# Optimization experiments

Measured on AMD Instinct MI355X. Metric: run time of the kernel, lower is better.

Reference implementation:

```python
import jax, jax.numpy as jnp
import numpy as np

ALPHA = 0.2  # LeakyReLU negative slope

B, K, F = 64, 100, 128   # batch, window_size (=num_nodes), n_features
E = 2 * K                 # embed_dim*2 = 200 (embed_dim defaults to window_size)


def setup_inputs() -> dict:
    key = jax.random.key(0)
    k1, k2, k3, k4, k5 = jax.random.split(key, 5)
    x = jax.random.normal(k1, (B, K, F), dtype=jnp.float32)
    # lin: Linear(2F -> E); store weight as (2F, E) so projection is x @ W
    W = jax.random.normal(k2, (2 * F, E), dtype=jnp.float32) * (1.0 / np.sqrt(2 * F))
    b = jax.random.normal(k3, (E,), dtype=jnp.float32) * 0.01
    # attention vector a: (E, 1) in torch; use (E,)
    a = jax.random.normal(k4, (E,), dtype=jnp.float32) * (1.414 / np.sqrt(E))
    bias = jax.random.normal(k5, (K, K), dtype=jnp.float32) * 0.01
    return {"x": x, "W": W, "b": b, "a": a, "bias": bias}


def reference(x, W, b, a, bias):
    F_ = x.shape[-1]
    # lin(concat(left, right)) == left @ W[:F] + right @ W[F:] + b;
    # compute the two projections once each instead of materializing the
    # (B, K, K, 2F) pairwise concat tensor.
    left_p = jnp.einsum('bkf,fe->bke', x, W[:F_])    # (B, K, E)
    right_p = jnp.einsum('bkf,fe->bke', x, W[F_:])   # (B, K, E)
    pre = left_p[:, :, None, :] + right_p[:, None, :, :] + b  # (B, K, K, E)
    act = jnp.where(pre > 0, pre, ALPHA * pre)                # LeakyReLU
    e = jnp.einsum('bije,e->bij', act, a) + bias              # (B, K, K)
    attention = jax.nn.softmax(e, axis=2)
    h = jax.nn.sigmoid(jnp.einsum('bij,bjf->bif', attention, x))  # (B, K, F)
    return h
```

## Files before the change

kernel.cpp:

```cpp
#include <hip/hip_runtime.h>

typedef _Float16 half_t;
typedef _Float16 h2 __attribute__((ext_vector_type(2)));
typedef unsigned int uint32;

#define K_ 100
#define F_ 128
#define E_ 200

#if defined(__has_builtin)
#if __has_builtin(__builtin_amdgcn_fdot2)
#define FDOT2(a,b,c) __builtin_amdgcn_fdot2((a),(b),(c),false)
#endif
#endif
#ifndef FDOT2
#define FDOT2(a,b,c) fmaf((float)(a).y,(float)(b).y, fmaf((float)(a).x,(float)(b).x,(c)))
#endif

__device__ __forceinline__ h2 bch2(uint32 u){ return __builtin_bit_cast(h2,u); }
__device__ __forceinline__ uint32 pkh2(float a, float b){
  h2 p; p.x=(half_t)a; p.y=(half_t)b; return __builtin_bit_cast(uint32,p);
}

#define LH_OFF 0
#define RH_OFF 640000
#define AH_OFF 1280000
#define WT_OFF 1280128
#define AL_OFF 1305728
#define AR_OFF 1312128
#define XJ_OFF 1318528

__global__ __launch_bounds__(256) void k_wt(
    const float* __restrict__ W, const float* __restrict__ avec,
    uint32* __restrict__ ws)
{
  const int t  = threadIdx.x;
  const int e0 = (int)blockIdx.x * 8;
  __shared__ float wtf[256 * 9];

  for (int u = t; u < 2048; u += 256) {
    int f = u >> 3, ec = u & 7;
    wtf[f * 9 + ec] = W[(size_t)f * E_ + e0 + ec];
  }
  if (blockIdx.x == 0 && t < 100)
    ws[AH_OFF + t] = pkh2(avec[2*t], avec[2*t+1]);
  __syncthreads();

  for (int u = t; u < 1024; u += 256) {
    int col16 = u >> 6, f2 = u & 63;
    int side = col16 >> 3, el = col16 & 7;
    int cu = side * 200 + e0 + el;
    int fbase = side * 128;
    ws[WT_OFF + (size_t)cu * 64 + f2] =
        pkh2(wtf[(fbase + 2*f2) * 9 + el], wtf[(fbase + 2*f2 + 1) * 9 + el]);
  }
}

__global__ __launch_bounds__(256) void k_proj(
    const float* __restrict__ x, const float* __restrict__ bvec,
    uint32* __restrict__ ws)
{
  const int t  = threadIdx.x;
  const int r0 = (int)blockIdx.x * 10;

  __shared__ __align__(16) uint32 xsh[10 * 64];
  __shared__ float red[20][100];

  for (int u = t; u < 640; u += 256) {
    int row = u >> 6, f2 = u & 63;
    const float* xp = x + (size_t)(r0 + row) * F_ + 2 * f2;
    xsh[row * 64 + f2] = pkh2(xp[0], xp[1]);
  }
  __syncthreads();

  for (int u = t; u < 640; u += 256) {
    int f = u & 127, lp = u >> 7;
    uint32 u0 = xsh[(2*lp)     * 64 + (f >> 1)];
    uint32 u1 = xsh[(2*lp + 1) * 64 + (f >> 1)];
    int sh = (f & 1) * 16;
    uint32 h0 = (u0 >> sh) & 0xffffu;
    uint32 h1 = (u1 >> sh) & 0xffffu;
    ws[XJ_OFF + (size_t)(r0/2 + lp) * 128 + f] = h0 | (h1 << 16);
  }

  if (t < 200) {
    const uint32* wt0 = ws + WT_OFF + (size_t)(2 * t) * 64;
    const uint32* wt1 = wt0 + 64;
    float acc0[10], acc1[10];
    #pragma unroll
    for (int r = 0; r < 10; ++r) { acc0[r] = 0.f; acc1[r] = 0.f; }
    #pragma unroll
    for (int q = 0; q < 16; ++q) {
      uint4 w0 = *(const uint4*)(wt0 + 4 * q);
      uint4 w1 = *(const uint4*)(wt1 + 4 * q);
      #pragma unroll
      for (int r = 0; r < 10; ++r) {
        uint4 xq = *(const uint4*)(xsh + r * 64 + 4 * q);
        acc0[r] = FDOT2(bch2(xq.x), bch2(w0.x), acc0[r]);
        acc0[r] = FDOT2(bch2(xq.y), bch2(w0.y), acc0[r]);
        acc0[r] = FDOT2(bch2(xq.z), bch2(w0.z), acc0[r]);
        acc0[r] = FDOT2(bch2(xq.w), bch2(w0.w), acc0[r]);
        acc1[r] = FDOT2(bch2(xq.x), bch2(w1.x), acc1[r]);
        acc1[r] = FDOT2(bch2(xq.y), bch2(w1.y), acc1[r]);
        acc1[r] = FDOT2(bch2(xq.z), bch2(w1.z), acc1[r]);
        acc1[r] = FDOT2(bch2(xq.w), bch2(w1.w), acc1[r]);
      }
    }
    const bool isR = (t >= 100);
    const int e2 = isR ? (t - 100) : t;
    if (isR) {
      float b0 = bvec[2 * e2], b1 = bvec[2 * e2 + 1];
      #pragma unroll
      for (int r = 0; r < 10; ++r) { acc0[r] += b0; acc1[r] += b1; }
    }
    h2 a2 = bch2(ws[AH_OFF + e2]);
    uint32* dst = ws + (isR ? RH_OFF : LH_OFF);
    #pragma unroll
    for (int r = 0; r < 10; ++r) {
      uint32 pr = pkh2(acc0[r], acc1[r]);
      dst[(size_t)(r0 + r) * 100 + e2] = pr;
      red[(isR ? 10 : 0) + r][e2] = FDOT2(a2, bch2(pr), 0.f);
    }
  }
  __syncthreads();

  if (t < 20) {
    float s = 0.f;
    const float* rp = red[t];
    for (int k = 0; k < 100; ++k) s += rp[k];
    float* dstf = (float*)(ws + (t >= 10 ? AR_OFF : AL_OFF));
    dstf[r0 + (t % 10)] = s;
  }
}

#define STEP(lu, au, r0u, r1u, r2u, r3u)                                   \
  do {                                                                     \
    h2 a2 = bch2(au); h2 l2 = bch2(lu); h2 mm;                             \
    mm = __builtin_elementwise_min(l2 + bch2(r0u), z2); acc[0] = FDOT2(a2, mm, acc[0]); \
    mm = __builtin_elementwise_min(l2 + bch2(r1u), z2); acc[1] = FDOT2(a2, mm, acc[1]); \
    mm = __builtin_elementwise_min(l2 + bch2(r2u), z2); acc[2] = FDOT2(a2, mm, acc[2]); \
    mm = __builtin_elementwise_min(l2 + bch2(r3u), z2); acc[3] = FDOT2(a2, mm, acc[3]); \
  } while (0)

#define RPAD 104
#define LPAD 108

__global__ __launch_bounds__(256) void k_main(
    const float* __restrict__ x, const float* __restrict__ bias,
    const uint32* __restrict__ ws, float* __restrict__ out)
{
  const int t  = threadIdx.x;
  const int i0 = (int)blockIdx.x * 10;
  const int b  = (int)blockIdx.y;

  __shared__ __align__(16) uint32 Rsh[100 * RPAD];
  __shared__ __align__(16) uint32 Lsh[10 * LPAD];
  __shared__ uint32 Ash[100];
  __shared__ float  att[10 * 100];
  __shared__ uint32 att2[10 * 50];
  __shared__ float  scratch[256];
  __shared__ float  rowmax[10], rowinv[10];

  const bool act = (t < 250);
  const int ti = act ? (t % 10) : 0;
  const int tj = act ? (t / 10) : 0;

  {
    const uint32* Rb = ws + RH_OFF + (size_t)b * K_ * 100;
    for (int u = t; u < 2500; u += 256) {
      int row = u / 25, c4 = (u % 25) * 4;
      *(uint4*)(&Rsh[row * RPAD + c4]) = *(const uint4*)(Rb + (size_t)row * 100 + c4);
    }
    const uint32* Lb = ws + LH_OFF + (size_t)(b * K_ + i0) * 100;
    if (t < 250) {
      int row = t / 25, c4 = (t % 25) * 4;
      *(uint4*)(&Lsh[row * LPAD + c4]) = *(const uint4*)(Lb + (size_t)row * 100 + c4);
    }
    if (t < 100) Ash[t] = ws[AH_OFF + t];
  }
  __syncthreads();

  float acc[4] = {0.f,0.f,0.f,0.f};
  h2 z2; z2.x = (half_t)0; z2.y = (half_t)0;

  if (act) {
    const uint32* Lp  = Lsh + ti * LPAD;
    const uint32* Rp0 = Rsh + tj * RPAD;
    const uint32* Rp1 = Rsh + (tj + 25) * RPAD;
    const uint32* Rp2 = Rsh + (tj + 50) * RPAD;
    const uint32* Rp3 = Rsh + (tj + 75) * RPAD;
    #pragma unroll 5
    for (int q = 0; q < 25; ++q) {
      uint4 Lq = *(const uint4*)(Lp  + 4*q);
      uint4 Aq = *(const uint4*)(Ash + 4*q);
      uint4 R0q = *(const uint4*)(Rp0 + 4*q);
      uint4 R1q = *(const uint4*)(Rp1 + 4*q);
      uint4 R2q = *(const uint4*)(Rp2 + 4*q);
      uint4 R3q = *(const uint4*)(Rp3 + 4*q);
      STEP(Lq.x, Aq.x, R0q.x, R1q.x, R2q.x, R3q.x);
      STEP(Lq.y, Aq.y, R0q.y, R1q.y, R2q.y, R3q.y);
      STEP(Lq.z, Aq.z, R0q.z, R1q.z, R2q.z, R3q.z);
      STEP(Lq.w, Aq.w, R0q.w, R1q.w, R2q.w, R3q.w);
    }
  }

  float v[4];
  if (act) {
    const float* ALf = (const float*)(ws + AL_OFF);
    const float* ARf = (const float*)(ws + AR_OFF);
    float al = ALf[b*K_ + i0 + ti];
    #pragma unroll
    for (int s = 0; s < 4; ++s) {
      int j = tj + 25*s;
      float lv = al + ARf[b*K_ + j] + bias[(i0 + ti)*K_ + j] - 0.8f*acc[s];
      v[s] = fminf(fmaxf(lv, -30000.f), 30000.f);
    }
  }

  {
    float m = -3.0e38f;
    if (act) {
      #pragma unroll
      for (int s = 0; s < 4; ++s) m = fmaxf(m, v[s]);
    }
    scratch[t] = m;
    __syncthreads();
    if (t < 10) {
      float mm = scratch[t];
      for (int k = 1; k < 25; ++k) mm = fmaxf(mm, scratch[t + 10*k]);
      rowmax[t] = mm;
    }
    __syncthreads();
    float ssum = 0.f;
    if (act) {
      float m2 = rowmax[ti];
      #pragma unroll
      for (int s = 0; s < 4; ++s) ssum += __expf(v[s] - m2);
    }
    scratch[t] = ssum;
    __syncthreads();
    if (t < 10) {
      float s2 = 0.f;
      for (int k = 0; k < 25; ++k) s2 += scratch[t + 10*k];
      rowinv[t] = 1.f / s2;
    }
    __syncthreads();
  }
  if (act) {
    float m = rowmax[ti], inv = rowinv[ti];
    #pragma unroll
    for (int s = 0; s < 4; ++s)
      att[ti*K_ + tj + 25*s] = __expf(v[s] - m) * inv;
  }
  __syncthreads();
  for (int u = t; u < 500; u += 256) {
    int i = u / 50, jp = u - i*50;
    att2[i*50 + jp] = pkh2(att[i*K_ + 2*jp], att[i*K_ + 2*jp + 1]);
  }
  __syncthreads();

  {
    const int f = t & 127, ig = t >> 7;
    const uint32* XJ = ws + XJ_OFF + (size_t)(b*50) * 128;
    float z[5];
    #pragma unroll
    for (int m = 0; m < 5; ++m) z[m] = 0.f;
    for (int jp = 0; jp < 50; ++jp) {
      h2 xv = bch2(XJ[jp*128 + f]);
      #pragma unroll
      for (int m = 0; m < 5; ++m) {
        h2 av = bch2(att2[(ig*5 + m)*50 + jp]);
        z[m] = FDOT2(av, xv, z[m]);
      }
    }
    #pragma unroll
    for (int m = 0; m < 5; ++m) {
      int i = ig*5 + m;
      out[(size_t)(b*K_ + i0 + i)*F_ + f] = 1.f / (1.f + __expf(-z[m]));
    }
  }
}

extern "C" void kernel_launch(void* const* d_in, const int* in_sizes, int n_in,
                              void* d_out, int out_size, void* d_ws, size_t ws_size,
                              hipStream_t stream)
{
  const float* x    = (const float*)d_in[0];
  const float* W    = (const float*)d_in[1];
  const float* bvec = (const float*)d_in[2];
  const float* avec = (const float*)d_in[3];
  const float* bias = (const float*)d_in[4];
  float* out  = (float*)d_out;
  uint32* ws  = (uint32*)d_ws;

  k_wt  <<<dim3(25),     dim3(256), 0, stream>>>(W, avec, ws);
  k_proj<<<dim3(640),    dim3(256), 0, stream>>>(x, bvec, ws);
  k_main<<<dim3(10, 64), dim3(256), 0, stream>>>(x, bias, ws, out);
}
```

Baseline: 101.8 us.

## Fuse weight prep, projection and attention into one persistent kernel with grid barrier

```diff
diff --git a/kernel.cpp b/kernel.cpp
--- a/kernel.cpp
+++ b/kernel.cpp
@@ -7,6 +7,7 @@
 #define K_ 100
 #define F_ 128
 #define E_ 200
+#define NBLK 640u
 
 #if defined(__has_builtin)
 #if __has_builtin(__builtin_amdgcn_fdot2)
@@ -22,115 +23,33 @@
   h2 p; p.x=(half_t)a; p.y=(half_t)b; return __builtin_bit_cast(uint32,p);
 }
 
-#define LH_OFF 0
-#define RH_OFF 640000
-#define AH_OFF 1280000
-#define WT_OFF 1280128
-#define AL_OFF 1305728
-#define AR_OFF 1312128
-#define XJ_OFF 1318528
-
-__global__ __launch_bounds__(256) void k_wt(
-    const float* __restrict__ W, const float* __restrict__ avec,
-    uint32* __restrict__ ws)
+#define RH_OFF  0
+#define AR_WOFF 640000
+#define XJ_WOFF 646400
+
+__device__ unsigned gbar_cnt = 0;
+__device__ unsigned gbar_gen = 0;
+
+__device__ __forceinline__ void grid_barrier()
 {
-  const int t  = threadIdx.x;
-  const int e0 = (int)blockIdx.x * 8;
-  __shared__ float wtf[256 * 9];
-
-  for (int u = t; u < 2048; u += 256) {
-    int f = u >> 3, ec = u & 7;
-    wtf[f * 9 + ec] = W[(size_t)f * E_ + e0 + ec];
-  }
-  if (blockIdx.x == 0 && t < 100)
-    ws[AH_OFF + t] = pkh2(avec[2*t], avec[2*t+1]);
-  __syncthreads();
-
-  for (int u = t; u < 1024; u += 256) {
-    int col16 = u >> 6, f2 = u & 63;
-    int side = col16 >> 3, el = col16 & 7;
-    int cu = side * 200 + e0 + el;
-    int fbase = side * 128;
-    ws[WT_OFF + (size_t)cu * 64 + f2] =
-        pkh2(wtf[(fbase + 2*f2) * 9 + el], wtf[(fbase + 2*f2 + 1) * 9 + el]);
-  }
-}
-
-__global__ __launch_bounds__(256) void k_proj(
-    const float* __restrict__ x, const float* __restrict__ bvec,
-    uint32* __restrict__ ws)
-{
-  const int t  = threadIdx.x;
-  const int r0 = (int)blockIdx.x * 10;
-
-  __shared__ __align__(16) uint32 xsh[10 * 64];
-  __shared__ float red[20][100];
-
-  for (int u = t; u < 640; u += 256) {
-    int row = u >> 6, f2 = u & 63;
-    const float* xp = x + (size_t)(r0 + row) * F_ + 2 * f2;
-    xsh[row * 64 + f2] = pkh2(xp[0], xp[1]);
-  }
-  __syncthreads();
-
-  for (int u = t; u < 640; u += 256) {
-    int f = u & 127, lp = u >> 7;
-    uint32 u0 = xsh[(2*lp)     * 64 + (f >> 1)];
-    uint32 u1 = xsh[(2*lp + 1) * 64 + (f >> 1)];
-    int sh = (f & 1) * 16;
-    uint32 h0 = (u0 >> sh) & 0xffffu;
-    uint32 h1 = (u1 >> sh) & 0xffffu;
-    ws[XJ_OFF + (size_t)(r0/2 + lp) * 128 + f] = h0 | (h1 << 16);
-  }
-
-  if (t < 200) {
-    const uint32* wt0 = ws + WT_OFF + (size_t)(2 * t) * 64;
-    const uint32* wt1 = wt0 + 64;
-    float acc0[10], acc1[10];
-    #pragma unroll
-    for (int r = 0; r < 10; ++r) { acc0[r] = 0.f; acc1[r] = 0.f; }
-    #pragma unroll
-    for (int q = 0; q < 16; ++q) {
-      uint4 w0 = *(const uint4*)(wt0 + 4 * q);
-      uint4 w1 = *(const uint4*)(wt1 + 4 * q);
-      #pragma unroll
-      for (int r = 0; r < 10; ++r) {
-        uint4 xq = *(const uint4*)(xsh + r * 64 + 4 * q);
-        acc0[r] = FDOT2(bch2(xq.x), bch2(w0.x), acc0[r]);
-        acc0[r] = FDOT2(bch2(xq.y), bch2(w0.y), acc0[r]);
-        acc0[r] = FDOT2(bch2(xq.z), bch2(w0.z), acc0[r]);
-        acc0[r] = FDOT2(bch2(xq.w), bch2(w0.w), acc0[r]);
-        acc1[r] = FDOT2(bch2(xq.x), bch2(w1.x), acc1[r]);
-        acc1[r] = FDOT2(bch2(xq.y), bch2(w1.y), acc1[r]);
-        acc1[r] = FDOT2(bch2(xq.z), bch2(w1.z), acc1[r]);
-        acc1[r] = FDOT2(bch2(xq.w), bch2(w1.w), acc1[r]);
-      }
-    }
-    const bool isR = (t >= 100);
-    const int e2 = isR ? (t - 100) : t;
-    if (isR) {
-      float b0 = bvec[2 * e2], b1 = bvec[2 * e2 + 1];
-      #pragma unroll
-      for (int r = 0; r < 10; ++r) { acc0[r] += b0; acc1[r] += b1; }
-    }
-    h2 a2 = bch2(ws[AH_OFF + e2]);
-    uint32* dst = ws + (isR ? RH_OFF : LH_OFF);
-    #pragma unroll
-    for (int r = 0; r < 10; ++r) {
-      uint32 pr = pkh2(acc0[r], acc1[r]);
-      dst[(size_t)(r0 + r) * 100 + e2] = pr;
-      red[(isR ? 10 : 0) + r][e2] = FDOT2(a2, bch2(pr), 0.f);
-    }
-  }
-  __syncthreads();
-
-  if (t < 20) {
-    float s = 0.f;
-    const float* rp = red[t];
-    for (int k = 0; k < 100; ++k) s += rp[k];
-    float* dstf = (float*)(ws + (t >= 10 ? AR_OFF : AL_OFF));
-    dstf[r0 + (t % 10)] = s;
-  }
+  __syncthreads();
+  if (threadIdx.x == 0) {
+    __threadfence();
+    unsigned g = __hip_atomic_load(&gbar_gen, __ATOMIC_RELAXED, __HIP_MEMORY_SCOPE_AGENT);
+    unsigned a = __hip_atomic_fetch_add(&gbar_cnt, 1u, __ATOMIC_ACQ_REL, __HIP_MEMORY_SCOPE_AGENT);
+    if (a == NBLK - 1u) {
+      __hip_atomic_store(&gbar_cnt, 0u, __ATOMIC_RELAXED, __HIP_MEMORY_SCOPE_AGENT);
+      __hip_atomic_fetch_add(&gbar_gen, 1u, __ATOMIC_RELEASE, __HIP_MEMORY_SCOPE_AGENT);
+    } else {
+      unsigned long long t0 = __builtin_amdgcn_s_memrealtime();
+      while (__hip_atomic_load(&gbar_gen, __ATOMIC_ACQUIRE, __HIP_MEMORY_SCOPE_AGENT) == g) {
+        __builtin_amdgcn_s_sleep(8);
+        if (__builtin_amdgcn_s_memrealtime() - t0 > 100000000ull) break;
+      }
+    }
+    __threadfence();
+  }
+  __syncthreads();
 }
 
 #define STEP(lu, au, r0u, r1u, r2u, r3u)                                   \
@@ -145,54 +64,132 @@
 #define RPAD 104
 #define LPAD 108
 
-__global__ __launch_bounds__(256) void k_main(
-    const float* __restrict__ x, const float* __restrict__ bias,
-    const uint32* __restrict__ ws, float* __restrict__ out)
+__global__ __launch_bounds__(256, 3) void k_fused(
+    const float* __restrict__ x, const float* __restrict__ W,
+    const float* __restrict__ bvec, const float* __restrict__ avec,
+    const float* __restrict__ bias, uint32* __restrict__ ws,
+    float* __restrict__ out)
 {
   const int t  = threadIdx.x;
-  const int i0 = (int)blockIdx.x * 10;
+  const int ib = (int)blockIdx.x;
   const int b  = (int)blockIdx.y;
-
-  __shared__ __align__(16) uint32 Rsh[100 * RPAD];
+  const int i0 = ib * 10;
+  const int r0 = b * K_ + i0;
+
+  __shared__ __align__(16) uint32 RshU[100 * RPAD];
   __shared__ __align__(16) uint32 Lsh[10 * LPAD];
-  __shared__ uint32 Ash[100];
-  __shared__ float  att[10 * 100];
+  __shared__ __align__(16) uint32 Ash[100];
+  __shared__ float  ALsh[12];
+  __shared__ __align__(16) float attU[10 * K_];
   __shared__ uint32 att2[10 * 50];
-  __shared__ float  scratch[256];
   __shared__ float  rowmax[10], rowinv[10];
 
-  const bool act = (t < 250);
-  const int ti = act ? (t % 10) : 0;
-  const int tj = act ? (t / 10) : 0;
+  uint32* xsh = RshU;
+  float*  red = (float*)(RshU + 640);
+  float*  scratch = attU;
+
+  for (int u = t; u < 640; u += 256) {
+    int row = u >> 6, f2 = u & 63;
+    const float* xp = x + (size_t)(r0 + row) * F_ + 2 * f2;
+    xsh[row * 64 + f2] = pkh2(xp[0], xp[1]);
+  }
+  if (t < 100) Ash[t] = pkh2(avec[2*t], avec[2*t+1]);
+  __syncthreads();
+
+  for (int u = t; u < 640; u += 256) {
+    int f = u & 127, lp = u >> 7;
+    uint32 u0 = xsh[(2*lp)     * 64 + (f >> 1)];
+    uint32 u1 = xsh[(2*lp + 1) * 64 + (f >> 1)];
+    int sh = (f & 1) * 16;
+    ws[XJ_WOFF + (size_t)(b*50 + ib*5 + lp) * 128 + f] =
+        ((u0 >> sh) & 0xffffu) | (((u1 >> sh) & 0xffffu) << 16);
+  }
+
+  if (t < 200) {
+    const bool isR = (t >= 100);
+    const int e2 = isR ? (t - 100) : t;
+    const float* Wp = W + (size_t)(isR ? 128 : 0) * E_ + 2 * e2;
+
+    float acc0[10], acc1[10];
+    #pragma unroll
+    for (int r = 0; r < 10; ++r) { acc0[r] = 0.f; acc1[r] = 0.f; }
+
+    #pragma unroll
+    for (int q = 0; q < 16; ++q) {
+      uint32 w0u[4], w1u[4];
+      #pragma unroll
+      for (int fp = 0; fp < 4; ++fp) {
+        const float* p0 = Wp + (size_t)(8*q + 2*fp) * E_;
+        float2 Av = *(const float2*)p0;
+        float2 Bv = *(const float2*)(p0 + E_);
+        w0u[fp] = pkh2(Av.x, Bv.x);
+        w1u[fp] = pkh2(Av.y, Bv.y);
+      }
+      #pragma unroll
+      for (int r = 0; r < 10; ++r) {
+        uint4 xq = *(const uint4*)(xsh + r * 64 + 4 * q);
+        acc0[r] = FDOT2(bch2(xq.x), bch2(w0u[0]), acc0[r]);
+        acc0[r] = FDOT2(bch2(xq.y), bch2(w0u[1]), acc0[r]);
+        acc0[r] = FDOT2(bch2(xq.z), bch2(w0u[2]), acc0[r]);
+        acc0[r] = FDOT2(bch2(xq.w), bch2(w0u[3]), acc0[r]);
+        acc1[r] = FDOT2(bch2(xq.x), bch2(w1u[0]), acc1[r]);
+        acc1[r] = FDOT2(bch2(xq.y), bch2(w1u[1]), acc1[r]);
+        acc1[r] = FDOT2(bch2(xq.z), bch2(w1u[2]), acc1[r]);
+        acc1[r] = FDOT2(bch2(xq.w), bch2(w1u[3]), acc1[r]);
+      }
+    }
+    if (isR) {
+      float b0 = bvec[2 * e2], b1 = bvec[2 * e2 + 1];
+      #pragma unroll
+      for (int r = 0; r < 10; ++r) { acc0[r] += b0; acc1[r] += b1; }
+    }
+    h2 a2 = bch2(Ash[e2]);
+    #pragma unroll
+    for (int r = 0; r < 10; ++r) {
+      uint32 pr = pkh2(acc0[r], acc1[r]);
+      if (isR) ws[RH_OFF + (size_t)(r0 + r) * 100 + e2] = pr;
+      else     Lsh[r * LPAD + e2] = pr;
+      red[(isR ? 10 : 0) * 100 + r * 100 + e2] = FDOT2(a2, bch2(pr), 0.f);
+    }
+  }
+  __syncthreads();
+
+  if (t < 20) {
+    float s = 0.f;
+    const float* rp = red + t * 100;
+    for (int k = 0; k < 100; ++k) s += rp[k];
+    if (t < 10) ALsh[t] = s;
+    else       ((float*)ws)[AR_WOFF + r0 + (t - 10)] = s;
+  }
+
+  grid_barrier();
 
   {
     const uint32* Rb = ws + RH_OFF + (size_t)b * K_ * 100;
     for (int u = t; u < 2500; u += 256) {
       int row = u / 25, c4 = (u % 25) * 4;
-      *(uint4*)(&Rsh[row * RPAD + c4]) = *(const uint4*)(Rb + (size_t)row * 100 + c4);
-    }
-    const uint32* Lb = ws + LH_OFF + (size_t)(b * K_ + i0) * 100;
-    if (t < 250) {
-      int row = t / 25, c4 = (t % 25) * 4;
-      *(uint4*)(&Lsh[row * LPAD + c4]) = *(const uint4*)(Lb + (size_t)row * 100 + c4);
-    }
-    if (t < 100) Ash[t] = ws[AH_OFF + t];
-  }
-  __syncthreads();
+      *(uint4*)(&RshU[row * RPAD + c4]) = *(const uint4*)(Rb + (size_t)row * 100 + c4);
+    }
+  }
+  __syncthreads();
+
+  const bool act = (t < 250);
+  const int ti = act ? (t % 10) : 0;
+  const int tj = act ? (t / 10) : 0;
 
   float acc[4] = {0.f,0.f,0.f,0.f};
   h2 z2; z2.x = (half_t)0; z2.y = (half_t)0;
 
   if (act) {
-    const uint32* Lp  = Lsh + ti * LPAD;
-    const uint32* Rp0 = Rsh + tj * RPAD;
-    const uint32* Rp1 = Rsh + (tj + 25) * RPAD;
-    const uint32* Rp2 = Rsh + (tj + 50) * RPAD;
-    const uint32* Rp3 = Rsh + (tj + 75) * RPAD;
+    const uint32* Lp  = Lsh  + ti * LPAD;
+    const uint32* Rp0 = RshU + tj * RPAD;
+    const uint32* Rp1 = RshU + (tj + 25) * RPAD;
+    const uint32* Rp2 = RshU + (tj + 50) * RPAD;
+    const uint32* Rp3 = RshU + (tj + 75) * RPAD;
     #pragma unroll 5
     for (int q = 0; q < 25; ++q) {
-      uint4 Lq = *(const uint4*)(Lp  + 4*q);
-      uint4 Aq = *(const uint4*)(Ash + 4*q);
+      uint4 Lq  = *(const uint4*)(Lp  + 4*q);
+      uint4 Aq  = *(const uint4*)(Ash + 4*q);
       uint4 R0q = *(const uint4*)(Rp0 + 4*q);
       uint4 R1q = *(const uint4*)(Rp1 + 4*q);
       uint4 R2q = *(const uint4*)(Rp2 + 4*q);
@@ -206,9 +203,8 @@
 
   float v[4];
   if (act) {
-    const float* ALf = (const float*)(ws + AL_OFF);
-    const float* ARf = (const float*)(ws + AR_OFF);
-    float al = ALf[b*K_ + i0 + ti];
+    const float* ARf = (const float*)ws + AR_WOFF;
+    float al = ALsh[ti];
     #pragma unroll
     for (int s = 0; s < 4; ++s) {
       int j = tj + 25*s;
@@ -250,18 +246,18 @@
     float m = rowmax[ti], inv = rowinv[ti];
     #pragma unroll
     for (int s = 0; s < 4; ++s)
-      att[ti*K_ + tj + 25*s] = __expf(v[s] - m) * inv;
+      attU[ti*K_ + tj + 25*s] = __expf(v[s] - m) * inv;
   }
   __syncthreads();
   for (int u = t; u < 500; u += 256) {
     int i = u / 50, jp = u - i*50;
-    att2[i*50 + jp] = pkh2(att[i*K_ + 2*jp], att[i*K_ + 2*jp + 1]);
+    att2[i*50 + jp] = pkh2(attU[i*K_ + 2*jp], attU[i*K_ + 2*jp + 1]);
   }
   __syncthreads();
 
   {
     const int f = t & 127, ig = t >> 7;
-    const uint32* XJ = ws + XJ_OFF + (size_t)(b*50) * 128;
+    const uint32* XJ = ws + XJ_WOFF + (size_t)(b*50) * 128;
     float z[5];
     #pragma unroll
     for (int m = 0; m < 5; ++m) z[m] = 0.f;
@@ -293,7 +289,5 @@
   float* out  = (float*)d_out;
   uint32* ws  = (uint32*)d_ws;
 
-  k_wt  <<<dim3(25),     dim3(256), 0, stream>>>(W, avec, ws);
-  k_proj<<<dim3(640),    dim3(256), 0, stream>>>(x, bvec, ws);
-  k_main<<<dim3(10, 64), dim3(256), 0, stream>>>(x, bias, ws, out);
-}
+  k_fused<<<dim3(10, 64), dim3(256), 0, stream>>>(x, W, bvec, avec, bias, ws, out);
+}
```

Result: slower. 231.9 us (+127.8%).
